# Performance work log

Hardware: AMD Instinct MI355X
Metric: run time of the kernel (lower is better)

The kernel has to match this reference:

```python
import jax, jax.numpy as jnp
import numpy as np

N, D, K = 524288, 256, 64
ALPHA = 1.0


def setup_inputs() -> dict:
    key = jax.random.key(0)
    k1, k2 = jax.random.split(key)
    inputs = jax.random.normal(k1, (N, D), dtype=jnp.float32)
    clusters = jax.random.normal(k2, (K, D), dtype=jnp.float32)  # glorot-init stand-in
    return {"inputs": inputs, "clusters": clusters}


def reference(inputs, clusters):
    # Squared euclidean distance ||x - c||^2 via GEMM expansion: same math as
    # sum((x[:,None,:] - c[None,:,:])**2, -1) without the (N,K,D) intermediate.
    x2 = jnp.sum(inputs * inputs, axis=1, keepdims=True)          # (N,1)
    c2 = jnp.sum(clusters * clusters, axis=1)                     # (K,)
    d2 = x2 + c2 - 2.0 * (inputs @ clusters.T)                    # (N,K)
    d2 = jnp.maximum(d2, 0.0)                                     # numeric guard
    q = 1.0 / (1.0 + d2 / ALPHA)                                  # Student-t kernel
    q = q ** ((ALPHA + 1.0) / 2.0)
    return q / jnp.sum(q, axis=1, keepdims=True)                  # row-normalize
```

## Files before the change

kernel.cpp:

```cpp
#include <hip/hip_runtime.h>
#include <hip/hip_bf16.h>

#define NPTS 524288
#define DIM 256
#define KC 64

typedef __attribute__((ext_vector_type(8))) short bf16x8;
typedef __attribute__((ext_vector_type(4))) float f32x4;

typedef __attribute__((address_space(1))) const unsigned int GUI;
typedef __attribute__((address_space(3))) unsigned int LUI;

static __device__ __forceinline__ void gload16(const void* g, void* l) {
  __builtin_amdgcn_global_load_lds((GUI*)g, (LUI*)l, 16, 0, 0);
}

static __device__ __forceinline__ ushort f32_to_bf16_rne(float f) {
  unsigned int b = __builtin_bit_cast(unsigned int, f);
  b += 0x7FFFu + ((b >> 16) & 1u);
  return (ushort)(b >> 16);
}

__global__ void prep_clusters(const float* __restrict__ C,
                              char* __restrict__ cb,
                              float* __restrict__ c2) {
  const int w = threadIdx.x >> 6;
  const int lane = threadIdx.x & 63;
  const int k = blockIdx.x * 8 + w * 2 + (lane >> 5);
  const int m = lane & 31;
  const float* src = C + k * DIM + m * 8;
  float4 u0 = ((const float4*)src)[0];
  float4 u1 = ((const float4*)src)[1];
  float vv[8] = {u0.x, u0.y, u0.z, u0.w, u1.x, u1.y, u1.z, u1.w};
  float s = 0.f;
  bf16x8 h;
#pragma unroll
  for (int j = 0; j < 8; ++j) {
    s = fmaf(vv[j], vv[j], s);
    h[j] = (short)f32_to_bf16_rne(vv[j]);
  }
  s += __shfl_xor(s, 1);
  s += __shfl_xor(s, 2);
  s += __shfl_xor(s, 4);
  s += __shfl_xor(s, 8);
  s += __shfl_xor(s, 16);
  const int slot = 16 * (k & 3) + (k >> 2);
  const int off = slot * 512 + ((m ^ (slot & 7)) << 4);
  *(bf16x8*)(cb + off) = h;
  if (m == 0) c2[k] = s;
}

__global__ __launch_bounds__(256, 2)
void cluster_q(const float* __restrict__ A, const char* __restrict__ cb,
               const float* __restrict__ c2, float* __restrict__ out) {
  __shared__ char lds[65536];
  const int tid = threadIdx.x;
  const int lane = tid & 63;
  const int w = tid >> 6;
  const int l15 = lane & 15;
  const int g = lane >> 4;
  const long brow = (long)blockIdx.x * 256;

  {
    const char* src = cb + w * 8192 + lane * 16;
    char* dst = lds + w * 8192;
#pragma unroll
    for (int i = 0; i < 8; ++i)
      gload16(src + i * 1024, dst + i * 1024);
  }

  const char* Abase = (const char*)A + (brow + w * 16) * 1024;

#define STAGE(ci)                                                            \
  do {                                                                       \
    char* dbase = lds + 32768 + w * 8192 + ((ci) & 1) * 4096;                \
    const char* sbase = Abase + ((ci) >> 2) * 65536 + ((ci) & 3) * 256;      \
    _Pragma("unroll") for (int c4 = 0; c4 < 4; ++c4) {                       \
      int o = c4 * 1024 + lane * 16;                                         \
      int row = o >> 8;                                                      \
      int swz = ((((o >> 4) & 15) ^ (row & 7)) << 4);                        \
      gload16(sbase + row * 1024 + swz, dbase + c4 * 1024);                  \
    }                                                                        \
  } while (0)

#define KSTEP(c, s2)                                                         \
  do {                                                                       \
    const char* abuf = lds + 32768 + w * 8192 + ((c) & 1) * 4096;            \
    int ga = (s2) * 8 + g * 2;                                               \
    int a0 = l15 * 256 + ((ga ^ (l15 & 7)) << 4);                            \
    float4 u0 = *(const float4*)(abuf + a0);                                 \
    float4 u1 = *(const float4*)(abuf + (a0 ^ 16));                          \
    float vv[8] = {u0.x, u0.y, u0.z, u0.w, u1.x, u1.y, u1.z, u1.w};          \
    bf16x8 af;                                                               \
    _Pragma("unroll") for (int j = 0; j < 8; ++j) {                          \
      x2l = fmaf(vv[j], vv[j], x2l);                                         \
      af[j] = (short)f32_to_bf16_rne(vv[j]);                                 \
    }                                                                        \
    int ks = ((c) & 3) * 2 + (s2);                                           \
    _Pragma("unroll") for (int t = 0; t < 4; ++t) {                          \
      int slot = l15 + 16 * t;                                               \
      bf16x8 bf = *(const bf16x8*)(lds + slot * 512 +                        \
                                   (((ks * 4 + g) ^ (slot & 7)) << 4));      \
      acc[t] = __builtin_amdgcn_mfma_f32_16x16x32_bf16(af, bf, acc[t], 0, 0, 0); \
    }                                                                        \
  } while (0)

#define CHUNK(c)                                                             \
  do {                                                                       \
    KSTEP(c, 0);                                                             \
    KSTEP(c, 1);                                                             \
    if ((c) + 2 < 16) STAGE((c) + 2);                                        \
  } while (0)

#define V0 asm volatile("s_waitcnt vmcnt(0)" ::: "memory")
#define V4 asm volatile("s_waitcnt vmcnt(4)" ::: "memory")
#define V8 asm volatile("s_waitcnt vmcnt(8)" ::: "memory")

#define INIT                                                                 \
  do {                                                                       \
    _Pragma("unroll") for (int t = 0; t < 4; ++t)                            \
        acc[t] = (f32x4){0.f, 0.f, 0.f, 0.f};                                \
    x2l = 0.f;                                                               \
  } while (0)

#define EPI(p)                                                               \
  do {                                                                       \
    x2l += __shfl_xor(x2l, 16);                                              \
    x2l += __shfl_xor(x2l, 32);                                              \
    float x2r[4];                                                            \
    _Pragma("unroll") for (int r = 0; r < 4; ++r)                            \
        x2r[r] = __shfl(x2l, g * 4 + r);                                     \
    float4 c2v = *(const float4*)(c2 + 4 * l15);                             \
    float c2a[4] = {c2v.x, c2v.y, c2v.z, c2v.w};                             \
    float qv[4][4];                                                          \
    float rsum[4] = {0.f, 0.f, 0.f, 0.f};                                    \
    _Pragma("unroll") for (int t = 0; t < 4; ++t) {                          \
      _Pragma("unroll") for (int r = 0; r < 4; ++r) {                        \
        float d2 = fmaxf(x2r[r] + c2a[t] - 2.0f * acc[t][r], 0.f);           \
        float qq = __builtin_amdgcn_rcpf(1.0f + d2);                         \
        qv[t][r] = qq;                                                       \
        rsum[r] += qq;                                                       \
      }                                                                      \
    }                                                                        \
    _Pragma("unroll") for (int r = 0; r < 4; ++r) {                          \
      rsum[r] += __shfl_xor(rsum[r], 1);                                     \
      rsum[r] += __shfl_xor(rsum[r], 2);                                     \
      rsum[r] += __shfl_xor(rsum[r], 4);                                     \
      rsum[r] += __shfl_xor(rsum[r], 8);                                     \
      float inv = __builtin_amdgcn_rcpf(rsum[r]);                            \
      long orow = brow + (p) * 64 + w * 16 + g * 4 + r;                      \
      float4 o4 = {qv[0][r] * inv, qv[1][r] * inv, qv[2][r] * inv,           \
                   qv[3][r] * inv};                                          \
      *(float4*)(out + orow * 64 + 4 * l15) = o4;                            \
    }                                                                        \
  } while (0)

  f32x4 acc[4];
  float x2l;

  STAGE(0);
  STAGE(1);
  __syncthreads();

  INIT;
        CHUNK(0);
        CHUNK(1);
   V4;  CHUNK(2);
   V4;  CHUNK(3);
  EPI(0);
  INIT;
   V8;  CHUNK(4);
   V8;  CHUNK(5);
   V4;  CHUNK(6);
   V4;  CHUNK(7);
  EPI(1);
  INIT;
   V8;  CHUNK(8);
   V8;  CHUNK(9);
  V4;  CHUNK(10);
  V4;  CHUNK(11);
  EPI(2);
  INIT;
  V8;  CHUNK(12);
  V8;  CHUNK(13);
  V4;  CHUNK(14);
  V0;  CHUNK(15);
  EPI(3);

#undef STAGE
#undef KSTEP
#undef CHUNK
#undef V0
#undef V4
#undef V8
#undef INIT
#undef EPI
}

extern "C" void kernel_launch(void* const* d_in, const int* in_sizes, int n_in,
                              void* d_out, int out_size, void* d_ws, size_t ws_size,
                              hipStream_t stream) {
  const float* inputs = (const float*)d_in[0];
  const float* clusters = (const float*)d_in[1];
  float* out = (float*)d_out;

  char* cb = (char*)d_ws;
  float* c2 = (float*)((char*)d_ws + 32768);

  prep_clusters<<<8, 256, 0, stream>>>(clusters, cb, c2);
  cluster_q<<<NPTS / 256, 256, 0, stream>>>(inputs, cb, c2, out);
}
```

Baseline: 140.9 us.

## Fuse cluster prep into main kernel and stream A via register prefetch

Removes the separate prep_clusters launch: each block now converts the clusters to bf16 in LDS itself and computes c2 into shared memory. A tiles are no longer staged through LDS with global_load_lds; instead each lane loads its fragment straight into registers with a rotating three-deep prefetch across k-steps. LDS use drops to about 33KB, allowing 4 blocks per CU, and each block handles 512 rows in a rolled loop. The trade-off is redundant cluster conversion in every block, uncoalesced row-strided direct loads, and higher register pressure.

```diff
diff --git a/kernel.cpp b/kernel.cpp
--- a/kernel.cpp
+++ b/kernel.cpp
@@ -8,129 +8,103 @@
 typedef __attribute__((ext_vector_type(8))) short bf16x8;
 typedef __attribute__((ext_vector_type(4))) float f32x4;
 
-typedef __attribute__((address_space(1))) const unsigned int GUI;
-typedef __attribute__((address_space(3))) unsigned int LUI;
-
-static __device__ __forceinline__ void gload16(const void* g, void* l) {
-  __builtin_amdgcn_global_load_lds((GUI*)g, (LUI*)l, 16, 0, 0);
+static __device__ __forceinline__ short f2bf(float f) {
+  return __builtin_bit_cast(short, __float2bfloat16(f));
 }
 
-static __device__ __forceinline__ ushort f32_to_bf16_rne(float f) {
-  unsigned int b = __builtin_bit_cast(unsigned int, f);
-  b += 0x7FFFu + ((b >> 16) & 1u);
-  return (ushort)(b >> 16);
-}
-
-__global__ void prep_clusters(const float* __restrict__ C,
-                              char* __restrict__ cb,
-                              float* __restrict__ c2) {
-  const int w = threadIdx.x >> 6;
-  const int lane = threadIdx.x & 63;
-  const int k = blockIdx.x * 8 + w * 2 + (lane >> 5);
-  const int m = lane & 31;
-  const float* src = C + k * DIM + m * 8;
-  float4 u0 = ((const float4*)src)[0];
-  float4 u1 = ((const float4*)src)[1];
-  float vv[8] = {u0.x, u0.y, u0.z, u0.w, u1.x, u1.y, u1.z, u1.w};
-  float s = 0.f;
-  bf16x8 h;
-#pragma unroll
-  for (int j = 0; j < 8; ++j) {
-    s = fmaf(vv[j], vv[j], s);
-    h[j] = (short)f32_to_bf16_rne(vv[j]);
-  }
-  s += __shfl_xor(s, 1);
-  s += __shfl_xor(s, 2);
-  s += __shfl_xor(s, 4);
-  s += __shfl_xor(s, 8);
-  s += __shfl_xor(s, 16);
-  const int slot = 16 * (k & 3) + (k >> 2);
-  const int off = slot * 512 + ((m ^ (slot & 7)) << 4);
-  *(bf16x8*)(cb + off) = h;
-  if (m == 0) c2[k] = s;
-}
-
-__global__ __launch_bounds__(256, 2)
-void cluster_q(const float* __restrict__ A, const char* __restrict__ cb,
-               const float* __restrict__ c2, float* __restrict__ out) {
-  __shared__ char lds[65536];
+__global__ __launch_bounds__(256, 4)
+void cluster_q(const float* __restrict__ A, const float* __restrict__ C,
+               float* __restrict__ out) {
+  __shared__ __align__(16) char lds[33024];
+  float* c2s = (float*)(lds + 32768);
   const int tid = threadIdx.x;
   const int lane = tid & 63;
   const int w = tid >> 6;
   const int l15 = lane & 15;
   const int g = lane >> 4;
-  const long brow = (long)blockIdx.x * 256;
+  const long blk = blockIdx.x;
+
+  const char* Ap = (const char*)A + blk * (512L * 1024) +
+                   (w * 16 + l15) * 1024 + g * 32;
+
+  float4 b0a = *(const float4*)(Ap + 0 * 128);
+  float4 b0b = *(const float4*)(Ap + 0 * 128 + 16);
+  float4 b1a = *(const float4*)(Ap + 1 * 128);
+  float4 b1b = *(const float4*)(Ap + 1 * 128 + 16);
+  float4 b2a = *(const float4*)(Ap + 2 * 128);
+  float4 b2b = *(const float4*)(Ap + 2 * 128 + 16);
+  float4 b3a, b3b;
 
   {
-    const char* src = cb + w * 8192 + lane * 16;
-    char* dst = lds + w * 8192;
+    const int k = tid >> 2;
+    const int qt = tid & 3;
+    const int slot = 16 * (k & 3) + (k >> 2);
+    const float4* src = (const float4*)(C + k * DIM + qt * 64);
+    float s = 0.f;
 #pragma unroll
-    for (int i = 0; i < 8; ++i)
-      gload16(src + i * 1024, dst + i * 1024);
+    for (int i = 0; i < 8; ++i) {
+      float4 u0 = src[2 * i];
+      float4 u1 = src[2 * i + 1];
+      float vv[8] = {u0.x, u0.y, u0.z, u0.w, u1.x, u1.y, u1.z, u1.w};
+      bf16x8 h;
+#pragma unroll
+      for (int j2 = 0; j2 < 8; ++j2) {
+        s = fmaf(vv[j2], vv[j2], s);
+        h[j2] = f2bf(vv[j2]);
+      }
+      const int m = qt * 8 + i;
+      *(bf16x8*)(lds + slot * 512 + ((m ^ (slot & 7)) << 4)) = h;
+    }
+    s += __shfl_xor(s, 1);
+    s += __shfl_xor(s, 2);
+    if (qt == 0) c2s[k] = s;
   }
+  __syncthreads();
 
-  const char* Abase = (const char*)A + (brow + w * 16) * 1024;
+  f32x4 acc[4];
+  float x2l;
 
-#define STAGE(ci)                                                            \
+#define KSTEP(ks, CA, CB, PA, PB, PF, pfa)                                   \
   do {                                                                       \
-    char* dbase = lds + 32768 + w * 8192 + ((ci) & 1) * 4096;                \
-    const char* sbase = Abase + ((ci) >> 2) * 65536 + ((ci) & 3) * 256;      \
-    _Pragma("unroll") for (int c4 = 0; c4 < 4; ++c4) {                       \
-      int o = c4 * 1024 + lane * 16;                                         \
-      int row = o >> 8;                                                      \
-      int swz = ((((o >> 4) & 15) ^ (row & 7)) << 4);                        \
-      gload16(sbase + row * 1024 + swz, dbase + c4 * 1024);                  \
+    float vv[8] = {CA.x, CA.y, CA.z, CA.w, CB.x, CB.y, CB.z, CB.w};          \
+    if (PF) {                                                                \
+      PA = *(const float4*)(pfa);                                            \
+      PB = *(const float4*)((pfa) + 16);                                     \
     }                                                                        \
-  } while (0)
-
-#define KSTEP(c, s2)                                                         \
-  do {                                                                       \
-    const char* abuf = lds + 32768 + w * 8192 + ((c) & 1) * 4096;            \
-    int ga = (s2) * 8 + g * 2;                                               \
-    int a0 = l15 * 256 + ((ga ^ (l15 & 7)) << 4);                            \
-    float4 u0 = *(const float4*)(abuf + a0);                                 \
-    float4 u1 = *(const float4*)(abuf + (a0 ^ 16));                          \
-    float vv[8] = {u0.x, u0.y, u0.z, u0.w, u1.x, u1.y, u1.z, u1.w};          \
     bf16x8 af;                                                               \
-    _Pragma("unroll") for (int j = 0; j < 8; ++j) {                          \
-      x2l = fmaf(vv[j], vv[j], x2l);                                         \
-      af[j] = (short)f32_to_bf16_rne(vv[j]);                                 \
+    _Pragma("unroll") for (int j2 = 0; j2 < 8; ++j2) {                       \
+      x2l = fmaf(vv[j2], vv[j2], x2l);                                       \
+      af[j2] = f2bf(vv[j2]);                                                 \
     }                                                                        \
-    int ks = ((c) & 3) * 2 + (s2);                                           \
     _Pragma("unroll") for (int t = 0; t < 4; ++t) {                          \
       int slot = l15 + 16 * t;                                               \
       bf16x8 bf = *(const bf16x8*)(lds + slot * 512 +                        \
-                                   (((ks * 4 + g) ^ (slot & 7)) << 4));      \
+                                   ((((ks) * 4 + g) ^ (slot & 7)) << 4));    \
       acc[t] = __builtin_amdgcn_mfma_f32_16x16x32_bf16(af, bf, acc[t], 0, 0, 0); \
     }                                                                        \
   } while (0)
 
-#define CHUNK(c)                                                             \
+#define CHUNK(j, NXT)                                                        \
   do {                                                                       \
-    KSTEP(c, 0);                                                             \
-    KSTEP(c, 1);                                                             \
-    if ((c) + 2 < 16) STAGE((c) + 2);                                        \
-  } while (0)
-
-#define V0 asm volatile("s_waitcnt vmcnt(0)" ::: "memory")
-#define V4 asm volatile("s_waitcnt vmcnt(4)" ::: "memory")
-#define V8 asm volatile("s_waitcnt vmcnt(8)" ::: "memory")
-
-#define INIT                                                                 \
-  do {                                                                       \
+    const char* ap = Ap + (j) * 65536;                                       \
+    const char* an = ap + 65536;                                             \
     _Pragma("unroll") for (int t = 0; t < 4; ++t)                            \
         acc[t] = (f32x4){0.f, 0.f, 0.f, 0.f};                                \
     x2l = 0.f;                                                               \
-  } while (0)
-
-#define EPI(p)                                                               \
-  do {                                                                       \
+    KSTEP(0, b0a, b0b, b3a, b3b, 1, ap + 3 * 128);                           \
+    KSTEP(1, b1a, b1b, b0a, b0b, 1, ap + 4 * 128);                           \
+    KSTEP(2, b2a, b2b, b1a, b1b, 1, ap + 5 * 128);                           \
+    KSTEP(3, b3a, b3b, b2a, b2b, 1, ap + 6 * 128);                           \
+    KSTEP(4, b0a, b0b, b3a, b3b, 1, ap + 7 * 128);                           \
+    KSTEP(5, b1a, b1b, b0a, b0b, NXT, an + 0 * 128);                         \
+    KSTEP(6, b2a, b2b, b1a, b1b, NXT, an + 1 * 128);                         \
+    KSTEP(7, b3a, b3b, b2a, b2b, NXT, an + 2 * 128);                         \
     x2l += __shfl_xor(x2l, 16);                                              \
     x2l += __shfl_xor(x2l, 32);                                              \
     float x2r[4];                                                            \
     _Pragma("unroll") for (int r = 0; r < 4; ++r)                            \
         x2r[r] = __shfl(x2l, g * 4 + r);                                     \
-    float4 c2v = *(const float4*)(c2 + 4 * l15);                             \
+    float4 c2v = *(const float4*)(c2s + 4 * l15);                            \
     float c2a[4] = {c2v.x, c2v.y, c2v.z, c2v.w};                             \
     float qv[4][4];                                                          \
     float rsum[4] = {0.f, 0.f, 0.f, 0.f};                                    \
@@ -148,53 +122,19 @@
       rsum[r] += __shfl_xor(rsum[r], 4);                                     \
       rsum[r] += __shfl_xor(rsum[r], 8);                                     \
       float inv = __builtin_amdgcn_rcpf(rsum[r]);                            \
-      long orow = brow + (p) * 64 + w * 16 + g * 4 + r;                      \
+      long orow = blk * 512 + (j) * 64 + w * 16 + g * 4 + r;                 \
       float4 o4 = {qv[0][r] * inv, qv[1][r] * inv, qv[2][r] * inv,           \
                    qv[3][r] * inv};                                          \
       *(float4*)(out + orow * 64 + 4 * l15) = o4;                            \
     }                                                                        \
   } while (0)
 
-  f32x4 acc[4];
-  float x2l;
+#pragma unroll 1
+  for (int j = 0; j < 7; ++j) CHUNK(j, 1);
+  CHUNK(7, 0);
 
-  STAGE(0);
-  STAGE(1);
-  __syncthreads();
-
-  INIT;
-        CHUNK(0);
-        CHUNK(1);
-   V4;  CHUNK(2);
-   V4;  CHUNK(3);
-  EPI(0);
-  INIT;
-   V8;  CHUNK(4);
-   V8;  CHUNK(5);
-   V4;  CHUNK(6);
-   V4;  CHUNK(7);
-  EPI(1);
-  INIT;
-   V8;  CHUNK(8);
-   V8;  CHUNK(9);
-  V4;  CHUNK(10);
-  V4;  CHUNK(11);
-  EPI(2);
-  INIT;
-  V8;  CHUNK(12);
-  V8;  CHUNK(13);
-  V4;  CHUNK(14);
-  V0;  CHUNK(15);
-  EPI(3);
-
-#undef STAGE
 #undef KSTEP
 #undef CHUNK
-#undef V0
-#undef V4
-#undef V8
-#undef INIT
-#undef EPI
 }
 
 extern "C" void kernel_launch(void* const* d_in, const int* in_sizes, int n_in,
@@ -203,10 +143,5 @@
   const float* inputs = (const float*)d_in[0];
   const float* clusters = (const float*)d_in[1];
   float* out = (float*)d_out;
-
-  char* cb = (char*)d_ws;
-  float* c2 = (float*)((char*)d_ws + 32768);
-
-  prep_clusters<<<8, 256, 0, stream>>>(clusters, cb, c2);
-  cluster_q<<<NPTS / 256, 256, 0, stream>>>(inputs, cb, c2, out);
+  cluster_q<<<NPTS / 512, 256, 0, stream>>>(inputs, clusters, out);
 }
```

After: 241.3 us. 1.71x slower.
